# Kernel tuning notes

Hardware: AMD Instinct MI355X
Metric: run time of the kernel (lower is better)

Reference implementation:

```python
import math
import jax, jax.numpy as jnp
import numpy as np

D_MODEL = 768
D_CROSS = 768
D_HEAD = 64
N_HEADS = D_MODEL // D_HEAD  # 12
D_FF = D_MODEL * 3           # 2304
EPS = 1e-6
N_FREQ = D_HEAD // 8         # freqs per axis (3 axes -> theta dim 24, rotates first 48 of 64 dims)


def make_rope_freqs():
    # k-diffusion style geometric frequencies in [pi, 10*pi), one table shared per head
    n = N_HEADS * N_FREQ
    f = np.exp(np.linspace(math.log(math.pi), math.log(10.0 * math.pi), n + 1)[:-1])
    return jnp.asarray(f.reshape(N_FREQ, N_HEADS).T, dtype=jnp.float32)  # [nh, N_FREQ]

ROPE_FREQS = make_rope_freqs()


def rms_norm(x, scale):
    ms = jnp.mean(jnp.square(x), axis=-1, keepdims=True)
    return x * (scale * jax.lax.rsqrt(ms + EPS))


def cos_scale(q, k, scale):
    # cosine-sim QK rescale: unit-normalize q,k per head then multiply by sqrt(learned scale)
    s = jnp.sqrt(scale)[:, None, None]  # [nh,1,1]
    q = q * (s * jax.lax.rsqrt(jnp.sum(jnp.square(q), -1, keepdims=True) + EPS))
    k = k * (s * jax.lax.rsqrt(jnp.sum(jnp.square(k), -1, keepdims=True) + EPS))
    return q, k


def rope_theta(pos):
    # pos [b,l,3] -> theta [b,nh,l,3*N_FREQ]
    b, l, _ = pos.shape
    th = pos[..., None, :, None] * ROPE_FREQS[:, None, :]  # [b,l,nh,3,N_FREQ]
    th = th.reshape(b, l, N_HEADS, 3 * N_FREQ)
    return jnp.swapaxes(th, 1, 2)  # movedim(-2,-3)


def apply_rope(x, theta):
    d = theta.shape[-1]
    x1, x2, x3 = x[..., :d], x[..., d:2 * d], x[..., 2 * d:]
    c, s = jnp.cos(theta), jnp.sin(theta)
    return jnp.concatenate([x1 * c - x2 * s, x2 * c + x1 * s, x3], axis=-1)


def sdpa(q, k, v):
    # scale=1.0 (cosine-sim already scaled)
    a = jax.nn.softmax(jnp.einsum('bhqe,bhke->bhqk', q, k), axis=-1)
    return jnp.einsum('bhqk,bhke->bhqe', a, v)


def reference(x, pos, x_cross, pos_cross,
              sa_norm_scale, sa_wqkv, sa_scale, sa_wout,
              ca_norm_scale, ca_norm_cross_scale, ca_wq, ca_wkv, ca_scale, ca_wout,
              ff_norm_scale, ff_wup, ff_wdown):
    b, l, _ = x.shape
    lc = x_cross.shape[1]

    # --- self attention ---
    h = rms_norm(x, sa_norm_scale)
    qkv = (h @ sa_wqkv.T).reshape(b, l, 3, N_HEADS, D_HEAD).transpose(2, 0, 3, 1, 4)
    q, k, v = qkv[0], qkv[1], qkv[2]  # [b,nh,l,e]
    q, k = cos_scale(q, k, sa_scale)
    theta = rope_theta(pos)
    q = apply_rope(q, theta)
    k = apply_rope(k, theta)
    o = sdpa(q, k, v)
    o = jnp.swapaxes(o, 1, 2).reshape(b, l, D_MODEL)
    x = o @ sa_wout.T + x

    # --- cross attention ---
    h = rms_norm(x, ca_norm_scale)
    hc = rms_norm(x_cross, ca_norm_cross_scale)
    q = (h @ ca_wq.T).reshape(b, l, N_HEADS, D_HEAD).transpose(0, 2, 1, 3)
    kv = (hc @ ca_wkv.T).reshape(b, lc, 2, N_HEADS, D_HEAD).transpose(2, 0, 3, 1, 4)
    k, v = kv[0], kv[1]
    q, k = cos_scale(q, k, ca_scale)
    q = apply_rope(q, rope_theta(pos))
    k = apply_rope(k, rope_theta(pos_cross))
    o = sdpa(q, k, v)
    o = jnp.swapaxes(o, 1, 2).reshape(b, l, D_MODEL)
    x = o @ ca_wout.T + x

    # --- SwiGLU FFN ---
    u = rms_norm(x, ff_norm_scale) @ ff_wup.T  # [b,l,2*d_ff]
    a, g = jnp.split(u, 2, axis=-1)
    x = (a * jax.nn.silu(g)) @ ff_wdown.T + x
    return x


def setup_inputs() -> dict:
    key = jax.random.key(0)
    ks = jax.random.split(key, 16)
    B, L = 2, 2048

    def w(k, out_f, in_f):
        return jax.random.normal(k, (out_f, in_f), dtype=jnp.float32) * (1.0 / math.sqrt(in_f))

    return {
        'x': jax.random.normal(ks[0], (B, L, D_MODEL), dtype=jnp.float32),
        'pos': jax.random.uniform(ks[1], (B, L, 3), dtype=jnp.float32),
        'x_cross': jax.random.normal(ks[2], (B, L, D_CROSS), dtype=jnp.float32),
        'pos_cross': jax.random.uniform(ks[3], (B, L, 3), dtype=jnp.float32),
        'sa_norm_scale': jnp.ones((D_MODEL,), jnp.float32),
        'sa_wqkv': w(ks[4], 3 * D_MODEL, D_MODEL),
        'sa_scale': jnp.full((N_HEADS,), 10.0, jnp.float32),
        'sa_wout': w(ks[5], D_MODEL, D_MODEL) * 0.02,
        'ca_norm_scale': jnp.ones((D_MODEL,), jnp.float32),
        'ca_norm_cross_scale': jnp.ones((D_CROSS,), jnp.float32),
        'ca_wq': w(ks[6], D_MODEL, D_MODEL),
        'ca_wkv': w(ks[7], 2 * D_MODEL, D_CROSS),
        'ca_scale': jnp.full((N_HEADS,), 10.0, jnp.float32),
        'ca_wout': w(ks[8], D_MODEL, D_MODEL) * 0.02,
        'ff_norm_scale': jnp.ones((D_MODEL,), jnp.float32),
        'ff_wup': w(ks[9], 2 * D_FF, D_MODEL),
        'ff_wdown': w(ks[10], D_MODEL, D_FF) * 0.02,
    }
```

## Files before the change

### kernel.cpp

```cpp
#include <hip/hip_runtime.h>
#include <hip/hip_bf16.h>
#include <math.h>

typedef __hip_bfloat16 bf16;

#define B 2
#define L 2048
#define DM 768
#define NH 12
#define DH 64
#define DFF 2304
#define M_TOK (B * L)

typedef __attribute__((ext_vector_type(8))) short bfrag;
typedef __attribute__((ext_vector_type(4))) float ffrag;
typedef __attribute__((ext_vector_type(16))) float facc16;

__device__ __forceinline__ float waveSum(float v) {
#pragma unroll
  for (int o = 32; o > 0; o >>= 1) v += __shfl_down(v, o, 64);
  return v;
}

__device__ __forceinline__ void gld16(void* l, const void* g) {
  __builtin_amdgcn_global_load_lds((const __attribute__((address_space(1))) unsigned*)g,
                                   (__attribute__((address_space(3))) unsigned*)l, 16, 0, 0);
}

#define BAR1_N(N) do { asm volatile("s_waitcnt vmcnt(" #N ")" ::: "memory"); \
                       __builtin_amdgcn_s_barrier(); } while (0)
#define BAR2() do { asm volatile("s_waitcnt lgkmcnt(0)" ::: "memory"); \
                    __builtin_amdgcn_s_barrier(); } while (0)

#define ASW(row, chunk) (((row) << 6) + ((((chunk) ^ ((row)&7))) << 3))

__global__ void k_castall(const float* __restrict__ s0, const float* __restrict__ s1,
                          const float* __restrict__ s2, const float* __restrict__ s3,
                          const float* __restrict__ s4, const float* __restrict__ s5,
                          const float* __restrict__ s6, bf16* __restrict__ dst) {
  const size_t DM2 = (size_t)DM * DM;
  size_t u = ((size_t)blockIdx.x * 256 + threadIdx.x) * 4;
  if (u >= 17 * DM2) return;
  const float* src;
  size_t loc;
  if (u < 3 * DM2) { src = s0; loc = u; }
  else if (u < 4 * DM2) { src = s1; loc = u - 3 * DM2; }
  else if (u < 5 * DM2) { src = s2; loc = u - 4 * DM2; }
  else if (u < 7 * DM2) { src = s3; loc = u - 5 * DM2; }
  else if (u < 8 * DM2) { src = s4; loc = u - 7 * DM2; }
  else if (u < 14 * DM2) { src = s5; loc = u - 8 * DM2; }
  else { src = s6; loc = u - 14 * DM2; }
  float4 v = *(const float4*)&src[loc];
  bf16* d = dst + u;
  d[0] = __float2bfloat16(v.x);
  d[1] = __float2bfloat16(v.y);
  d[2] = __float2bfloat16(v.z);
  d[3] = __float2bfloat16(v.w);
}

__global__ __launch_bounds__(256) void k_rmsnorm(const float* __restrict__ in,
                                                 const float* __restrict__ scale,
                                                 bf16* __restrict__ out) {
  int row = blockIdx.x;
  int t = threadIdx.x;
  const float* r = in + (size_t)row * DM;
  float x0 = r[t], x1 = r[t + 256], x2 = r[t + 512];
  float ss = x0 * x0 + x1 * x1 + x2 * x2;
  ss = waveSum(ss);
  __shared__ float red[4];
  int w = t >> 6, ln = t & 63;
  if (ln == 0) red[w] = ss;
  __syncthreads();
  float tot = red[0] + red[1] + red[2] + red[3];
  float g = rsqrtf(tot / (float)DM + 1e-6f);
  bf16* o = out + (size_t)row * DM;
  o[t] = __float2bfloat16(x0 * g * scale[t]);
  o[t + 256] = __float2bfloat16(x1 * g * scale[t + 256]);
  o[t + 512] = __float2bfloat16(x2 * g * scale[t + 512]);
}

template <int NT, int OBF>
__global__ __launch_bounds__(256) void k_gemm(const bf16* __restrict__ A,
                                              const bf16* __restrict__ W,
                                              float* __restrict__ C,
                                              bf16* __restrict__ Cb,
                                              const float* __restrict__ res,
                                              int M, int N, int K) {
  __shared__ __align__(16) bf16 As[2 * 128 * 64];
  __shared__ __align__(16) bf16 Bs[2 * NT * 64];
  const int t = threadIdx.x;
  const int w = t >> 6, lane = t & 63;
  const int m0 = blockIdx.y * 128, n0 = blockIdx.x * NT;
  const int quad = lane >> 4, l16 = lane & 15;
  constexpr int MI = (NT == 128) ? 4 : 2;
  const int wrow = (NT == 128) ? (w >> 1) * 64 : w * 32;
  const int wcol = (NT == 128) ? (w & 1) * 64 : 0;

  ffrag acc[MI][4];
#pragma unroll
  for (int i = 0; i < MI; i++)
#pragma unroll
    for (int j = 0; j < 4; j++) acc[i][j] = (ffrag){0.f, 0.f, 0.f, 0.f};

  const bf16 *pA[4], *pB[4];
  int lA[4], lB[4];
#pragma unroll
  for (int it = 0; it < 4; it++) {
    int lc = (w * 4 + it) * 64 + lane;
    int r = lc >> 3, c = lc & 7, kc = c ^ (r & 7);
    pA[it] = A + (size_t)(m0 + r) * K + kc * 8;
    lA[it] = lc * 8;
  }
  if (NT == 128) {
#pragma unroll
    for (int it = 0; it < 4; it++) {
      int lc = (w * 4 + it) * 64 + lane;
      int r = lc >> 3, c = lc & 7, kc = c ^ (r & 7);
      pB[it] = W + (size_t)(n0 + r) * K + kc * 8;
      lB[it] = lc * 8;
    }
  } else {
#pragma unroll
    for (int it = 0; it < 2; it++) {
      int lc = (w * 2 + it) * 64 + lane;
      int r = lc >> 3, c = lc & 7, kc = c ^ (r & 7);
      pB[it] = W + (size_t)(n0 + r) * K + kc * 8;
      lB[it] = lc * 8;
    }
  }
  auto stage = [&](int sel) {
#pragma unroll
    for (int it = 0; it < 4; it++) { gld16(&As[sel * 8192 + lA[it]], pA[it]); pA[it] += 64; }
    if (NT == 128) {
#pragma unroll
      for (int it = 0; it < 4; it++) { gld16(&Bs[sel * 8192 + lB[it]], pB[it]); pB[it] += 64; }
    } else {
#pragma unroll
      for (int it = 0; it < 2; it++) { gld16(&Bs[sel * 4096 + lB[it]], pB[it]); pB[it] += 64; }
    }
  };

  const int NK = K >> 6;
  stage(0);
  for (int kt = 0; kt < NK; kt++) {
    int cur = kt & 1;
    if (kt + 1 < NK) {
      stage(cur ^ 1);
      if constexpr (NT == 128) { BAR1_N(8); } else { BAR1_N(6); }
    } else {
      BAR1_N(0);
    }
    const bf16* Ab = As + cur * 8192;
    const bf16* Bb = Bs + cur * (NT == 128 ? 8192 : 4096);
#pragma unroll
    for (int s = 0; s < 2; s++) {
      bfrag af[MI], bfv[4];
#pragma unroll
      for (int i = 0; i < MI; i++)
        af[i] = *(const bfrag*)&Ab[ASW(wrow + i * 16 + l16, s * 4 + quad)];
#pragma unroll
      for (int j = 0; j < 4; j++)
        bfv[j] = *(const bfrag*)&Bb[ASW(wcol + j * 16 + l16, s * 4 + quad)];
#pragma unroll
      for (int i = 0; i < MI; i++)
#pragma unroll
        for (int j = 0; j < 4; j++)
          acc[i][j] = __builtin_amdgcn_mfma_f32_16x16x32_bf16(af[i], bfv[j], acc[i][j], 0, 0, 0);
    }
    BAR2();
  }
#pragma unroll
  for (int i = 0; i < MI; i++) {
    int mrow = m0 + wrow + i * 16 + quad * 4;
#pragma unroll
    for (int j = 0; j < 4; j++) {
      int ncol = n0 + wcol + j * 16 + l16;
#pragma unroll
      for (int r = 0; r < 4; r++) {
        float v = acc[i][j][r];
        size_t idx = (size_t)(mrow + r) * N + ncol;
        if (OBF) {
          Cb[idx] = __float2bfloat16(v);
        } else {
          if (res) v += res[idx];
          C[idx] = v;
        }
      }
    }
  }
}

__global__ __launch_bounds__(256) void k_ffup(const bf16* __restrict__ A,
                                              const bf16* __restrict__ Wup,
                                              bf16* __restrict__ Out) {
  __shared__ __align__(16) bf16 As[2 * 128 * 64];
  __shared__ __align__(16) bf16 Ba[2 * 64 * 64];
  __shared__ __align__(16) bf16 Bg[2 * 64 * 64];
  const int t = threadIdx.x, w = t >> 6, lane = t & 63;
  const int m0 = blockIdx.y * 128, n0 = blockIdx.x * 64;
  const int quad = lane >> 4, l16 = lane & 15;

  ffrag aa[2][4], ag[2][4];
#pragma unroll
  for (int i = 0; i < 2; i++)
#pragma unroll
    for (int j = 0; j < 4; j++) {
      aa[i][j] = (ffrag){0.f, 0.f, 0.f, 0.f};
      ag[i][j] = (ffrag){0.f, 0.f, 0.f, 0.f};
    }

  const bf16 *pA[4], *pBa[2], *pBg[2];
  int lA[4], lB[2];
#pragma unroll
  for (int it = 0; it < 4; it++) {
    int lc = (w * 4 + it) * 64 + lane;
    int r = lc >> 3, c = lc & 7, kc = c ^ (r & 7);
    pA[it] = A + (size_t)(m0 + r) * DM + kc * 8;
    lA[it] = lc * 8;
  }
#pragma unroll
  for (int it = 0; it < 2; it++) {
    int lc = (w * 2 + it) * 64 + lane;
    int r = lc >> 3, c = lc & 7, kc = c ^ (r & 7);
    pBa[it] = Wup + (size_t)(n0 + r) * DM + kc * 8;
    pBg[it] = Wup + (size_t)(DFF + n0 + r) * DM + kc * 8;
    lB[it] = lc * 8;
  }
  auto stage = [&](int sel) {
#pragma unroll
    for (int it = 0; it < 4; it++) { gld16(&As[sel * 8192 + lA[it]], pA[it]); pA[it] += 64; }
#pragma unroll
    for (int it = 0; it < 2; it++) {
      gld16(&Ba[sel * 4096 + lB[it]], pBa[it]); pBa[it] += 64;
      gld16(&Bg[sel * 4096 + lB[it]], pBg[it]); pBg[it] += 64;
    }
  };

  const int NK = DM / 64;
  stage(0);
  for (int kt = 0; kt < NK; kt++) {
    int cur = kt & 1;
    if (kt + 1 < NK) {
      stage(cur ^ 1);
      BAR1_N(8);
    } else {
      BAR1_N(0);
    }
    const bf16* Ab = As + cur * 8192;
    const bf16* Bab = Ba + cur * 4096;
    const bf16* Bgb = Bg + cur * 4096;
#pragma unroll
    for (int s = 0; s < 2; s++) {
      bfrag af[2], ba[4], bg[4];
#pragma unroll
      for (int i = 0; i < 2; i++)
        af[i] = *(const bfrag*)&Ab[ASW(w * 32 + i * 16 + l16, s * 4 + quad)];
#pragma unroll
      for (int j = 0; j < 4; j++) {
        ba[j] = *(const bfrag*)&Bab[ASW(j * 16 + l16, s * 4 + quad)];
        bg[j] = *(const bfrag*)&Bgb[ASW(j * 16 + l16, s * 4 + quad)];
      }
#pragma unroll
      for (int i = 0; i < 2; i++)
#pragma unroll
        for (int j = 0; j < 4; j++) {
          aa[i][j] = __builtin_amdgcn_mfma_f32_16x16x32_bf16(af[i], ba[j], aa[i][j], 0, 0, 0);
          ag[i][j] = __builtin_amdgcn_mfma_f32_16x16x32_bf16(af[i], bg[j], ag[i][j], 0, 0, 0);
        }
    }
    BAR2();
  }
#pragma unroll
  for (int i = 0; i < 2; i++) {
    int mrow = m0 + w * 32 + i * 16 + quad * 4;
#pragma unroll
    for (int j = 0; j < 4; j++) {
      int ncol = n0 + j * 16 + l16;
#pragma unroll
      for (int r = 0; r < 4; r++) {
        float a = aa[i][j][r], g = ag[i][j][r];
        float v = a * g / (1.f + __expf(-g));
        Out[(size_t)(mrow + r) * DFF + ncol] = __float2bfloat16(v);
      }
    }
  }
}

__device__ __forceinline__ void rope8(const bf16* __restrict__ inp, const float* __restrict__ pos3,
                                      float s, float fr0, int k, int lane,
                                      bf16* __restrict__ outp) {
  bfrag v = *(const bfrag*)inp;
  float x[8];
#pragma unroll
  for (int i = 0; i < 8; i++) x[i] = __bfloat162float(__builtin_bit_cast(bf16, (short)v[i]));
  float ss = 0.f;
#pragma unroll
  for (int i = 0; i < 8; i++) ss += x[i] * x[i];
  ss += __shfl_xor(ss, 1, 64);
  ss += __shfl_xor(ss, 2, 64);
  ss += __shfl_xor(ss, 4, 64);
  float g = s * rsqrtf(ss + 1e-6f);
#pragma unroll
  for (int i = 0; i < 8; i++) x[i] *= g;
  int pk = k < 3 ? k + 3 : (k < 6 ? k - 3 : k);
  int psrc = (lane & 56) | pk;
  float other[8];
#pragma unroll
  for (int i = 0; i < 8; i++) other[i] = __shfl(x[i], psrc, 64);
  bfrag o;
  if (k < 6) {
    int c = k < 3 ? k : k - 3;
    float p = pos3[c];
    float fr = fr0;
    float sgn = k < 3 ? -1.f : 1.f;
#pragma unroll
    for (int i = 0; i < 8; i++) {
      float th = p * fr;
      fr *= 1.333521432163324f;
      float st = __sinf(th), ct = __cosf(th);
      o[i] = __builtin_bit_cast(short, __float2bfloat16(x[i] * ct + sgn * other[i] * st));
    }
  } else {
#pragma unroll
    for (int i = 0; i < 8; i++) o[i] = __builtin_bit_cast(short, __float2bfloat16(x[i]));
  }
  *(bfrag*)outp = o;
}

__global__ __launch_bounds__(256) void k_ropeqk(const bf16* __restrict__ inQ, int strQ, int offQ,
                                                const bf16* __restrict__ inK, int strK, int offK,
                                                const float* __restrict__ posQ,
                                                const float* __restrict__ posK,
                                                const float* __restrict__ scale,
                                                bf16* __restrict__ outQ, bf16* __restrict__ outK) {
  int wid = blockIdx.x * 4 + (threadIdx.x >> 6);
  int lane = threadIdx.x & 63;
  int k = lane & 7;
  int item = wid * 8 + (lane >> 3);
  int l = item % L;
  int bh = item / L;
  int h = bh % NH;
  int b = bh / NH;
  float s = sqrtf(scale[h]);
  float fr0 = __expf(1.14472988584940017f + (float)h * 0.023985261385354646f);
  size_t tokrow = (size_t)(b * L + l);
  rope8(inQ + tokrow * strQ + offQ + h * DH + k * 8, &posQ[tokrow * 3], s, fr0, k, lane,
        outQ + (size_t)item * DH + k * 8);
  rope8(inK + tokrow * strK + offK + h * DH + k * 8, &posK[tokrow * 3], s, fr0, k, lane,
        outK + (size_t)item * DH + k * 8);
}

__global__ __launch_bounds__(256) void k_vtrans(const bf16* __restrict__ in, int stride, int off,
                                                bf16* __restrict__ Vt) {
  __shared__ __align__(16) bf16 St[64 * 64];
  int lt = blockIdx.x & 31, bh = blockIdx.x >> 5;
  int h = bh % NH, b = bh / NH;
  int t = threadIdx.x;
#pragma unroll
  for (int pass = 0; pass < 2; pass++) {
    int cid = t + pass * 256;
    int r = cid >> 3, c = cid & 7;
    *(float4*)&St[ASW(r, c)] =
        *(const float4*)&in[(size_t)(b * L + lt * 64 + r) * stride + off + h * DH + c * 8];
  }
  __syncthreads();
  const short* Ss = (const short*)St;
#pragma unroll
  for (int pass = 0; pass < 2; pass++) {
    int cid = t + pass * 256;
    int d = cid >> 3, oc = cid & 7;
    bfrag tmp;
#pragma unroll
    for (int i = 0; i < 8; i++) {
      int p = oc * 8 + i;
      int tok = (p & ~12) | ((p & 4) << 1) | ((p & 8) >> 1);
      tmp[i] = Ss[(tok << 6) + ((((d >> 3) ^ (tok & 7))) << 3) + (d & 7)];
    }
    *(bfrag*)&Vt[((size_t)bh * DH + d) * L + lt * 64 + oc * 8] = tmp;
  }
}

__global__ __launch_bounds__(256) void k_attn_mfma(const bf16* __restrict__ Q,
                                                   const bf16* __restrict__ K,
                                                   const bf16* __restrict__ Vt,
                                                   const float* __restrict__ scale,
                                                   bf16* __restrict__ O) {
  __shared__ __align__(16) char smem[32768 + 512];
  bf16* Ks = (bf16*)smem;
  bf16* Vs = (bf16*)(smem + 16384);
  float* Oex = (float*)smem;
  float* Lred = (float*)(smem + 32768);
  int qt = blockIdx.x & 31, bh = blockIdx.x >> 5;
  int h = bh % NH, b = bh / NH;
  float smax = scale[h];
  float nsl2 = -smax * 1.442695040888963f;
  int t = threadIdx.x, w = t >> 6, lane = t & 63;
  int hh = lane >> 5, l32 = lane & 31;
  int qsub = w >> 1, ksub = w & 1;

  const bf16* kbase = K + (size_t)(bh * L) * DH;
  const bf16* vbase = Vt + (size_t)bh * DH * L;

  const bf16* qrow = Q + ((size_t)(bh * L) + qt * 64 + qsub * 32 + l32) * DH;
  bfrag qf[4];
#pragma unroll
  for (int c = 0; c < 4; c++) qf[c] = *(const bfrag*)&qrow[c * 16 + hh * 8];

  facc16 o0, o1;
#pragma unroll
  for (int i = 0; i < 16; i++) { o0[i] = 0.f; o1[i] = 0.f; }
  float l_run = 0.f;

  const bf16 *kg0, *kg1, *vg0, *vg1;
  int lk0, lk1;
  {
    int r0 = w * 8 + (lane >> 3);
    int kc0 = (lane & 7) ^ (r0 & 7);
    int r1 = r0 + 32;
    int kc1 = (lane & 7) ^ (r1 & 7);
    kg0 = kbase + (size_t)r0 * DH + kc0 * 8;
    kg1 = kbase + (size_t)r1 * DH + kc1 * 8;
    vg0 = vbase + (size_t)r0 * L + kc0 * 8;
    vg1 = vbase + (size_t)r1 * L + kc1 * 8;
    lk0 = (w * 8) * 64 + lane * 8;
    lk1 = (w * 8 + 32) * 64 + lane * 8;
  }
  auto stageKV = [&](int sel) {
    gld16(&Ks[sel * 4096 + lk0], kg0); kg0 += 64 * DH;
    gld16(&Ks[sel * 4096 + lk1], kg1); kg1 += 64 * DH;
    gld16(&Vs[sel * 4096 + lk0], vg0); vg0 += 64;
    gld16(&Vs[sel * 4096 + lk1], vg1); vg1 += 64;
  };

  stageKV(0);
  for (int kt = 0; kt < 32; kt++) {
    int cur = kt & 1;
    if (kt < 31) {
      stageKV(cur ^ 1);
      BAR1_N(4);
    } else {
      BAR1_N(0);
    }
    const bf16* Kb = Ks + cur * 4096;
    const bf16* Vb = Vs + cur * 4096;
    facc16 s;
#pragma unroll
    for (int i = 0; i < 16; i++) s[i] = 0.f;
#pragma unroll
    for (int c = 0; c < 4; c++) {
      bfrag kf = *(const bfrag*)&Kb[ASW(ksub * 32 + l32, c * 2 + hh)];
      s = __builtin_amdgcn_mfma_f32_32x32x16_bf16(kf, qf[c], s, 0, 0, 0);
    }
    float pv[16];
#pragma unroll
    for (int reg = 0; reg < 16; reg++) {
      float p = __builtin_amdgcn_exp2f(__builtin_fmaf(s[reg], 1.442695040888963f, nsl2));
      l_run += p;
      pv[reg] = p;
    }
    bfrag pf0, pf1;
#pragma unroll
    for (int j = 0; j < 8; j++) {
      pf0[j] = __builtin_bit_cast(short, __float2bfloat16(pv[j]));
      pf1[j] = __builtin_bit_cast(short, __float2bfloat16(pv[8 + j]));
    }
    {
      bfrag vf;
      vf = *(const bfrag*)&Vb[ASW(l32, ksub * 4 + hh)];
      o0 = __builtin_amdgcn_mfma_f32_32x32x16_bf16(pf0, vf, o0, 0, 0, 0);
      vf = *(const bfrag*)&Vb[ASW(l32, ksub * 4 + 2 + hh)];
      o0 = __builtin_amdgcn_mfma_f32_32x32x16_bf16(pf1, vf, o0, 0, 0, 0);
      vf = *(const bfrag*)&Vb[ASW(32 + l32, ksub * 4 + hh)];
      o1 = __builtin_amdgcn_mfma_f32_32x32x16_bf16(pf0, vf, o1, 0, 0, 0);
      vf = *(const bfrag*)&Vb[ASW(32 + l32, ksub * 4 + 2 + hh)];
      o1 = __builtin_amdgcn_mfma_f32_32x32x16_bf16(pf1, vf, o1, 0, 0, 0);
    }
    BAR2();
  }
  l_run += __shfl_xor(l_run, 32, 64);
  __syncthreads();
  {
    int gd = (ksub ^ 1) * 32 + l32;
#pragma unroll
    for (int reg = 0; reg < 16; reg++) {
      int row = (reg & 3) + 8 * (reg >> 2) + 4 * hh;
      float gv = ksub ? o0[reg] : o1[reg];
      Oex[(size_t)(qsub * 32 + row) * 64 + gd] = gv;
    }
  }
  if (lane < 32) Lred[ksub * 64 + qsub * 32 + lane] = l_run;
  __syncthreads();
  {
    int d = ksub * 32 + l32;
#pragma unroll
    for (int reg = 0; reg < 16; reg++) {
      int row = (reg & 3) + 8 * (reg >> 2) + 4 * hh;
      int qg2 = qsub * 32 + row;
      float ltot = Lred[qg2] + Lred[64 + qg2];
      float keep = ksub ? o1[reg] : o0[reg];
      float v = (keep + Oex[(size_t)qg2 * 64 + d]) / ltot;
      O[(((size_t)(b * L) + qt * 64 + qg2) * NH + h) * DH + d] = __float2bfloat16(v);
    }
  }
}

extern "C" void kernel_launch(void* const* d_in, const int* in_sizes, int n_in,
                              void* d_out, int out_size, void* d_ws, size_t ws_size,
                              hipStream_t stream) {
  const float* x = (const float*)d_in[0];
  const float* pos = (const float*)d_in[1];
  const float* x_cross = (const float*)d_in[2];
  const float* pos_cross = (const float*)d_in[3];
  const float* sa_norm_scale = (const float*)d_in[4];
  const float* sa_wqkv = (const float*)d_in[5];
  const float* sa_scale = (const float*)d_in[6];
  const float* sa_wout = (const float*)d_in[7];
  const float* ca_norm_scale = (const float*)d_in[8];
  const float* ca_norm_cross_scale = (const float*)d_in[9];
  const float* ca_wq = (const float*)d_in[10];
  const float* ca_wkv = (const float*)d_in[11];
  const float* ca_scale = (const float*)d_in[12];
  const float* ca_wout = (const float*)d_in[13];
  const float* ff_norm_scale = (const float*)d_in[14];
  const float* ff_wup = (const float*)d_in[15];
  const float* ff_wdown = (const float*)d_in[16];
  float* out = (float*)d_out;

  float* ws = (float*)d_ws;
  const size_t S = (size_t)M_TOK * DM;
  float* xbuf = ws;
  bf16* b16 = (bf16*)(ws + S);
  bf16* qkvb = b16;
  bf16* qb = b16 + 3 * S;
  bf16* kb = b16 + 4 * S;
  bf16* vtb = b16 + 5 * S;
  bf16* hb = b16 + 6 * S;
  bf16* hcb = b16 + 7 * S;
  bf16* obb = b16 + 8 * S;
  bf16* wqkvb = b16 + 9 * S;
  bf16* woutb = wqkvb + (size_t)3 * DM * DM;
  bf16* wqb = woutb + (size_t)DM * DM;
  bf16* wkvb = wqb + (size_t)DM * DM;
  bf16* wout2b = wkvb + (size_t)2 * DM * DM;
  bf16* wupb = wout2b + (size_t)DM * DM;
  bf16* wdownb = wupb + (size_t)2 * DFF * DM;
  bf16* ffb = qkvb;

  const int ropeGrid = B * NH * L / 32;
  const int attnGrid = B * NH * (L / 64);
  const int vtGrid = B * NH * (L / 64);
  const size_t DM2 = (size_t)DM * DM;
  const int castGrid = (int)((17 * DM2 / 4 + 255) / 256);

  k_castall<<<castGrid, 256, 0, stream>>>(sa_wqkv, sa_wout, ca_wq, ca_wkv, ca_wout, ff_wup,
                                          ff_wdown, wqkvb);

  k_rmsnorm<<<M_TOK, 256, 0, stream>>>(x_cross, ca_norm_cross_scale, hcb);

  k_rmsnorm<<<M_TOK, 256, 0, stream>>>(x, sa_norm_scale, hb);
  k_gemm<128, 1><<<dim3(3 * DM / 128, M_TOK / 128), 256, 0, stream>>>(
      hb, wqkvb, nullptr, qkvb, nullptr, M_TOK, 3 * DM, DM);
  k_ropeqk<<<ropeGrid, 256, 0, stream>>>(qkvb, 3 * DM, 0, qkvb, 3 * DM, DM, pos, pos, sa_scale,
                                         qb, kb);
  k_vtrans<<<vtGrid, 256, 0, stream>>>(qkvb, 3 * DM, 2 * DM, vtb);
  k_attn_mfma<<<attnGrid, 256, 0, stream>>>(qb, kb, vtb, sa_scale, obb);
  k_gemm<64, 0><<<dim3(DM / 64, M_TOK / 128), 256, 0, stream>>>(
      obb, woutb, xbuf, nullptr, x, M_TOK, DM, DM);

  k_rmsnorm<<<M_TOK, 256, 0, stream>>>(xbuf, ca_norm_scale, hb);
  k_gemm<64, 1><<<dim3(DM / 64, M_TOK / 128), 256, 0, stream>>>(
      hb, wqb, nullptr, qkvb, nullptr, M_TOK, DM, DM);
  k_gemm<128, 1><<<dim3(2 * DM / 128, M_TOK / 128), 256, 0, stream>>>(
      hcb, wkvb, nullptr, qkvb + S, nullptr, M_TOK, 2 * DM, DM);
  k_ropeqk<<<ropeGrid, 256, 0, stream>>>(qkvb, DM, 0, qkvb + S, 2 * DM, 0, pos, pos_cross,
                                         ca_scale, qb, kb);
  k_vtrans<<<vtGrid, 256, 0, stream>>>(qkvb + S, 2 * DM, DM, vtb);
  k_attn_mfma<<<attnGrid, 256, 0, stream>>>(qb, kb, vtb, ca_scale, obb);
  k_gemm<64, 0><<<dim3(DM / 64, M_TOK / 128), 256, 0, stream>>>(
      obb, wout2b, xbuf, nullptr, xbuf, M_TOK, DM, DM);

  k_rmsnorm<<<M_TOK, 256, 0, stream>>>(xbuf, ff_norm_scale, hb);
  k_ffup<<<dim3(DFF / 64, M_TOK / 128), 256, 0, stream>>>(hb, wupb, ffb);
  k_gemm<64, 0><<<dim3(DM / 64, M_TOK / 128), 256, 0, stream>>>(
      ffb, wdownb, out, nullptr, xbuf, M_TOK, DM, DFF);
}
```

Before: 435.6 us.

## Triple-buffer attention K/V, shrink FF-up K tile, merge two RMSNorm launches

The attention kernel moves from a double-buffered to a triple-buffered K/V ring and drops the trailing barrier per iteration, so loads run two tiles ahead and one sync per step is saved. The FF-up GEMM now uses a K tile of 32 instead of 64, with a new swizzle, halving its shared memory and possibly raising occupancy at the cost of more loop iterations and barriers. The two input RMSNorm launches are merged into one kernel. The larger attention shared-memory footprint may lower occupancy there, and the single barrier with a three-buffer ring leaves little margin for a race.

```diff
diff --git a/kernel.cpp b/kernel.cpp
--- a/kernel.cpp
+++ b/kernel.cpp
@@ -58,11 +58,9 @@
   d[3] = __float2bfloat16(v.w);
 }
 
-__global__ __launch_bounds__(256) void k_rmsnorm(const float* __restrict__ in,
-                                                 const float* __restrict__ scale,
-                                                 bf16* __restrict__ out) {
-  int row = blockIdx.x;
-  int t = threadIdx.x;
+__device__ __forceinline__ void rms_body(const float* __restrict__ in,
+                                         const float* __restrict__ scale, int row, int t,
+                                         bf16* __restrict__ out) {
   const float* r = in + (size_t)row * DM;
   float x0 = r[t], x1 = r[t + 256], x2 = r[t + 512];
   float ss = x0 * x0 + x1 * x1 + x2 * x2;
@@ -77,6 +75,23 @@
   o[t] = __float2bfloat16(x0 * g * scale[t]);
   o[t + 256] = __float2bfloat16(x1 * g * scale[t + 256]);
   o[t + 512] = __float2bfloat16(x2 * g * scale[t + 512]);
+}
+
+__global__ __launch_bounds__(256) void k_rmsnorm(const float* __restrict__ in,
+                                                 const float* __restrict__ scale,
+                                                 bf16* __restrict__ out) {
+  rms_body(in, scale, blockIdx.x, threadIdx.x, out);
+}
+
+__global__ __launch_bounds__(256) void k_rmsnorm2(const float* __restrict__ in0,
+                                                  const float* __restrict__ sc0,
+                                                  bf16* __restrict__ out0,
+                                                  const float* __restrict__ in1,
+                                                  const float* __restrict__ sc1,
+                                                  bf16* __restrict__ out1) {
+  int row = blockIdx.x;
+  if (row < M_TOK) rms_body(in0, sc0, row, threadIdx.x, out0);
+  else rms_body(in1, sc1, row - M_TOK, threadIdx.x, out1);
 }
 
 template <int NT, int OBF>
@@ -193,9 +208,9 @@
 __global__ __launch_bounds__(256) void k_ffup(const bf16* __restrict__ A,
                                               const bf16* __restrict__ Wup,
                                               bf16* __restrict__ Out) {
-  __shared__ __align__(16) bf16 As[2 * 128 * 64];
-  __shared__ __align__(16) bf16 Ba[2 * 64 * 64];
-  __shared__ __align__(16) bf16 Bg[2 * 64 * 64];
+  __shared__ __align__(16) bf16 As[2 * 128 * 32];
+  __shared__ __align__(16) bf16 Ba[2 * 64 * 32];
+  __shared__ __align__(16) bf16 Bg[2 * 64 * 32];
   const int t = threadIdx.x, w = t >> 6, lane = t & 63;
   const int m0 = blockIdx.y * 128, n0 = blockIdx.x * 64;
   const int quad = lane >> 4, l16 = lane & 15;
@@ -209,65 +224,61 @@
       ag[i][j] = (ffrag){0.f, 0.f, 0.f, 0.f};
     }
 
-  const bf16 *pA[4], *pBa[2], *pBg[2];
-  int lA[4], lB[2];
-#pragma unroll
-  for (int it = 0; it < 4; it++) {
-    int lc = (w * 4 + it) * 64 + lane;
-    int r = lc >> 3, c = lc & 7, kc = c ^ (r & 7);
-    pA[it] = A + (size_t)(m0 + r) * DM + kc * 8;
-    lA[it] = lc * 8;
-  }
-#pragma unroll
-  for (int it = 0; it < 2; it++) {
-    int lc = (w * 2 + it) * 64 + lane;
-    int r = lc >> 3, c = lc & 7, kc = c ^ (r & 7);
-    pBa[it] = Wup + (size_t)(n0 + r) * DM + kc * 8;
-    pBg[it] = Wup + (size_t)(DFF + n0 + r) * DM + kc * 8;
-    lB[it] = lc * 8;
+  const bf16 *pA0, *pA1, *pBa, *pBg;
+  int lA0, lA1, lBc;
+  {
+    int lc0 = (w * 2 + 0) * 64 + lane;
+    int r0 = lc0 >> 2, kc0 = (lc0 & 3) ^ ((r0 >> 1) & 3);
+    int lc1 = (w * 2 + 1) * 64 + lane;
+    int r1 = lc1 >> 2, kc1 = (lc1 & 3) ^ ((r1 >> 1) & 3);
+    pA0 = A + (size_t)(m0 + r0) * DM + kc0 * 8; lA0 = lc0 * 8;
+    pA1 = A + (size_t)(m0 + r1) * DM + kc1 * 8; lA1 = lc1 * 8;
+    int lc = w * 64 + lane;
+    int r = lc >> 2, kc = (lc & 3) ^ ((r >> 1) & 3);
+    pBa = Wup + (size_t)(n0 + r) * DM + kc * 8;
+    pBg = Wup + (size_t)(DFF + n0 + r) * DM + kc * 8;
+    lBc = lc * 8;
   }
   auto stage = [&](int sel) {
-#pragma unroll
-    for (int it = 0; it < 4; it++) { gld16(&As[sel * 8192 + lA[it]], pA[it]); pA[it] += 64; }
-#pragma unroll
-    for (int it = 0; it < 2; it++) {
-      gld16(&Ba[sel * 4096 + lB[it]], pBa[it]); pBa[it] += 64;
-      gld16(&Bg[sel * 4096 + lB[it]], pBg[it]); pBg[it] += 64;
-    }
+    gld16(&As[sel * 4096 + lA0], pA0); pA0 += 32;
+    gld16(&As[sel * 4096 + lA1], pA1); pA1 += 32;
+    gld16(&Ba[sel * 2048 + lBc], pBa); pBa += 32;
+    gld16(&Bg[sel * 2048 + lBc], pBg); pBg += 32;
   };
 
-  const int NK = DM / 64;
+  const int NK = DM / 32;
   stage(0);
   for (int kt = 0; kt < NK; kt++) {
     int cur = kt & 1;
     if (kt + 1 < NK) {
       stage(cur ^ 1);
-      BAR1_N(8);
+      BAR1_N(4);
     } else {
       BAR1_N(0);
     }
-    const bf16* Ab = As + cur * 8192;
-    const bf16* Bab = Ba + cur * 4096;
-    const bf16* Bgb = Bg + cur * 4096;
-#pragma unroll
-    for (int s = 0; s < 2; s++) {
-      bfrag af[2], ba[4], bg[4];
-#pragma unroll
-      for (int i = 0; i < 2; i++)
-        af[i] = *(const bfrag*)&Ab[ASW(w * 32 + i * 16 + l16, s * 4 + quad)];
+    const bf16* Ab = As + cur * 4096;
+    const bf16* Bab = Ba + cur * 2048;
+    const bf16* Bgb = Bg + cur * 2048;
+    bfrag af[2], ba[4], bg[4];
+#pragma unroll
+    for (int i = 0; i < 2; i++) {
+      int r = w * 32 + i * 16 + l16;
+      af[i] = *(const bfrag*)&Ab[r * 32 + (quad ^ ((r >> 1) & 3)) * 8];
+    }
+#pragma unroll
+    for (int j = 0; j < 4; j++) {
+      int r = j * 16 + l16;
+      int sw = (quad ^ ((r >> 1) & 3)) * 8;
+      ba[j] = *(const bfrag*)&Bab[r * 32 + sw];
+      bg[j] = *(const bfrag*)&Bgb[r * 32 + sw];
+    }
+#pragma unroll
+    for (int i = 0; i < 2; i++)
 #pragma unroll
       for (int j = 0; j < 4; j++) {
-        ba[j] = *(const bfrag*)&Bab[ASW(j * 16 + l16, s * 4 + quad)];
-        bg[j] = *(const bfrag*)&Bgb[ASW(j * 16 + l16, s * 4 + quad)];
+        aa[i][j] = __builtin_amdgcn_mfma_f32_16x16x32_bf16(af[i], ba[j], aa[i][j], 0, 0, 0);
+        ag[i][j] = __builtin_amdgcn_mfma_f32_16x16x32_bf16(af[i], bg[j], ag[i][j], 0, 0, 0);
       }
-#pragma unroll
-      for (int i = 0; i < 2; i++)
-#pragma unroll
-        for (int j = 0; j < 4; j++) {
-          aa[i][j] = __builtin_amdgcn_mfma_f32_16x16x32_bf16(af[i], ba[j], aa[i][j], 0, 0, 0);
-          ag[i][j] = __builtin_amdgcn_mfma_f32_16x16x32_bf16(af[i], bg[j], ag[i][j], 0, 0, 0);
-        }
-    }
     BAR2();
   }
 #pragma unroll
@@ -385,11 +396,11 @@
                                                    const bf16* __restrict__ Vt,
                                                    const float* __restrict__ scale,
                                                    bf16* __restrict__ O) {
-  __shared__ __align__(16) char smem[32768 + 512];
+  __shared__ __align__(16) char smem[49152 + 512];
   bf16* Ks = (bf16*)smem;
-  bf16* Vs = (bf16*)(smem + 16384);
+  bf16* Vs = (bf16*)(smem + 24576);
   float* Oex = (float*)smem;
-  float* Lred = (float*)(smem + 32768);
+  float* Lred = (float*)(smem + 49152);
   int qt = blockIdx.x & 31, bh = blockIdx.x >> 5;
   int h = bh % NH, b = bh / NH;
   float smax = scale[h];
@@ -433,13 +444,13 @@
   };
 
   stageKV(0);
+  stageKV(1);
+  int cur = 0;
   for (int kt = 0; kt < 32; kt++) {
-    int cur = kt & 1;
-    if (kt < 31) {
-      stageKV(cur ^ 1);
-      BAR1_N(4);
-    } else {
-      BAR1_N(0);
+    if (kt < 31) { BAR1_N(4); } else { BAR1_N(0); }
+    if (kt + 2 < 32) {
+      int nb = cur + 2; if (nb >= 3) nb -= 3;
+      stageKV(nb);
     }
     const bf16* Kb = Ks + cur * 4096;
     const bf16* Vb = Vs + cur * 4096;
@@ -475,7 +486,7 @@
       vf = *(const bfrag*)&Vb[ASW(32 + l32, ksub * 4 + 2 + hh)];
       o1 = __builtin_amdgcn_mfma_f32_32x32x16_bf16(pf1, vf, o1, 0, 0, 0);
     }
-    BAR2();
+    cur = (cur == 2) ? 0 : cur + 1;
   }
   l_run += __shfl_xor(l_run, 32, 64);
   __syncthreads();
@@ -555,9 +566,9 @@
   k_castall<<<castGrid, 256, 0, stream>>>(sa_wqkv, sa_wout, ca_wq, ca_wkv, ca_wout, ff_wup,
                                           ff_wdown, wqkvb);
 
-  k_rmsnorm<<<M_TOK, 256, 0, stream>>>(x_cross, ca_norm_cross_scale, hcb);
-
-  k_rmsnorm<<<M_TOK, 256, 0, stream>>>(x, sa_norm_scale, hb);
+  k_rmsnorm2<<<2 * M_TOK, 256, 0, stream>>>(x, sa_norm_scale, hb, x_cross, ca_norm_cross_scale,
+                                            hcb);
+
   k_gemm<128, 1><<<dim3(3 * DM / 128, M_TOK / 128), 256, 0, stream>>>(
       hb, wqkvb, nullptr, qkvb, nullptr, M_TOK, 3 * DM, DM);
   k_ropeqk<<<ropeGrid, 256, 0, stream>>>(qkvb, 3 * DM, 0, qkvb, 3 * DM, DM, pos, pos, sa_scale,
```

Result: no change. 431.3 us (-1.0%).
